# Kernel tuning notes

Hardware: AMD Instinct MI355X
Metric: run time of the kernel (lower is better)

## Reference

```python
import jax, jax.numpy as jnp
import numpy as np

NV = [156, 618, 2466]     # vertices per ellipsoid level
NE = [462, 1848, 7392]    # edges per level
NGT = 30000               # ground-truth point-cloud size
LAP_CONST = [0.2, 1.0, 1.0]


def setup_inputs() -> dict:
    key = jax.random.key(0)
    ks = jax.random.split(key, 20)
    inp = {"points": jax.random.normal(ks[0], (1, NGT, 3), jnp.float32)}
    for i, (n, e) in enumerate(zip(NV, NE)):
        inp[f"pred_coord_{i}"] = jax.random.normal(ks[1 + i], (n, 3), jnp.float32)
        inp[f"pbd_{i}"] = jax.random.normal(ks[4 + i], (n, 3), jnp.float32)
        inp[f"edges_{i}"] = jax.random.randint(ks[7 + i], (e, 2), 0, n)
        # laplace_idx layout: 8 neighbor ids (-1 padded), vertex id, valence
        nbr = jax.random.randint(ks[10 + i], (n, 8), 0, n)
        drop = jax.random.uniform(ks[13 + i], (n, 8)) < 0.2
        drop = drop.at[:, 0].set(False)  # keep valence >= 1
        nbr = jnp.where(drop, -1, nbr)
        deg = (nbr >= 0).sum(1)
        inp[f"lap_idx_{i}"] = jnp.concatenate(
            [nbr, jnp.arange(n)[:, None], deg[:, None]], axis=1)
    return inp


def chamfer(gt, pred):
    # gt: [B, Ng, 3], pred: [B, Np, 3] -> squared NN distances each way
    d = (jnp.sum(gt * gt, -1)[:, :, None]
         + jnp.sum(pred * pred, -1)[:, None, :]
         - 2.0 * jnp.einsum('bnd,bmd->bnm', gt, pred))  # [B, Ng, Np]
    return jnp.min(d, axis=2), jnp.min(d, axis=1)


def edge_regularization(pred, edges):
    edge = pred[edges[:, 0]] - pred[edges[:, 1]]
    return jnp.mean(jnp.sum(edge * edge, axis=1)) * 300.0


def laplace_coord(x, lap_idx):
    nbr = lap_idx[:, :8]
    valid = nbr >= 0
    v = jnp.where(valid[:, :, None], x[jnp.clip(nbr, 0)], 0.0)  # [N, 8, 3]
    deg = lap_idx[:, -1].astype(x.dtype)
    return x - v.sum(1) / deg[:, None]


def laplace_regularization(x_before, x_after, lap_idx, use_move):
    lap1 = laplace_coord(x_before, lap_idx)
    lap2 = laplace_coord(x_after, lap_idx)
    d = lap1 - lap2
    loss = jnp.mean(d * d) * 3.0  # MSE over [N,3] scaled by last dim
    if use_move:
        m = x_before - x_after
        loss = loss + jnp.mean(m * m) * 3.0
    return loss


def reference(points, pred_coord_0, pred_coord_1, pred_coord_2,
              pbd_0, pbd_1, pbd_2,
              edges_0, edges_1, edges_2,
              lap_idx_0, lap_idx_1, lap_idx_2):
    pred_coord = [pred_coord_0, pred_coord_1, pred_coord_2]
    pbd = [pbd_0, pbd_1, pbd_2]
    edges = [edges_0, edges_1, edges_2]
    lap_idx = [lap_idx_0, lap_idx_1, lap_idx_2]

    chamfer_loss = 0.0
    edge_loss = 0.0
    lap_loss = 0.0
    for i in range(3):
        dist1, dist2 = chamfer(points, pbd[i][None])
        chamfer_loss = chamfer_loss + jnp.mean(dist1) + jnp.mean(dist2)
        edge_loss = edge_loss + edge_regularization(pred_coord[i], edges[i])
        lap_loss = lap_loss + LAP_CONST[i] * laplace_regularization(
            pbd[i], pred_coord[i], lap_idx[i], i > 0)
    loss = 100.0 * chamfer_loss + 0.1 * edge_loss + 0.3 * lap_loss
    return loss, chamfer_loss, edge_loss, lap_loss
```

## Files before the change

kernel.cpp:

```cpp
#include <hip/hip_runtime.h>

#define NGT 30000
#define GT_TILE 1024
#define NBLK_G 30
#define CHUNK 128
#define NCHUNK 27
#define RB 128

__global__ __launch_bounds__(256) void chamfer_kernel(
    const float* __restrict__ gt,
    const float* __restrict__ pbd0,
    const float* __restrict__ pbd1,
    const float* __restrict__ pbd2,
    float* __restrict__ gtmin,
    float* __restrict__ predmin)
{
    __shared__ float4 sgt[GT_TILE];
    __shared__ float4 spred[CHUNK];

    const int tid = threadIdx.x;
    const int c = blockIdx.y;

    int mesh, cidx;
    if (c < 2)      { mesh = 0; cidx = c; }
    else if (c < 7) { mesh = 1; cidx = c - 2; }
    else            { mesh = 2; cidx = c - 7; }
    const int coff = cidx * CHUNK;
    const int n    = (mesh == 0) ? 156 : (mesh == 1) ? 618 : 2466;
    const int poff = (mesh == 0) ? 0   : (mesh == 1) ? 156 : 774;
    const float* pred = (mesh == 0) ? pbd0 : (mesh == 1) ? pbd1 : pbd2;
    const int np = min(CHUNK, n - coff);

    if (tid < CHUNK) {
        float4 v = make_float4(0.f, 0.f, 0.f, 0.f);
        if (tid < np) {
            const int j = coff + tid;
            float px = pred[3*j], py = pred[3*j+1], pz = pred[3*j+2];
            v = make_float4(px, py, pz, px*px + py*py + pz*pz);
        }
        spred[tid] = v;
    }

    const int gbase = blockIdx.x * GT_TILE;
    float gx[4], gy[4], gz[4], g2[4], gmin[4];
    #pragma unroll
    for (int k = 0; k < 4; ++k) {
        const int g = gbase + k * 256 + tid;
        float x = 1e18f, y = 1e18f, z = 1e18f;
        if (g < NGT) { x = gt[3*g]; y = gt[3*g+1]; z = gt[3*g+2]; }
        gx[k] = x; gy[k] = y; gz[k] = z;
        g2[k] = x*x + y*y + z*z;
        gmin[k] = 3.0e38f;
        sgt[k * 256 + tid] = make_float4(x, y, z, g2[k]);
    }
    __syncthreads();

    #pragma unroll 2
    for (int j = 0; j < np; ++j) {
        const float4 p = spred[j];
        #pragma unroll
        for (int k = 0; k < 4; ++k) {
            float dot = gx[k]*p.x + gy[k]*p.y + gz[k]*p.z;
            float t = __fmaf_rn(dot, -2.0f, p.w);
            gmin[k] = fminf(gmin[k], t);
        }
    }
    #pragma unroll
    for (int k = 0; k < 4; ++k) {
        const int g = gbase + k * 256 + tid;
        if (g < NGT)
            atomicMin((int*)(gtmin + mesh * NGT + g),
                      __float_as_int(gmin[k] + g2[k]));
    }

    {
        const int grp = tid >> 3;
        const int s   = tid & 7;
        float4 p[4];
        #pragma unroll
        for (int r = 0; r < 4; ++r) p[r] = spred[4*grp + r];
        float mn[4] = {3.0e38f, 3.0e38f, 3.0e38f, 3.0e38f};
        #pragma unroll 2
        for (int k = 0; k < GT_TILE / 8; ++k) {
            const float4 q = sgt[k * 8 + s];
            #pragma unroll
            for (int r = 0; r < 4; ++r) {
                float dot = q.x*p[r].x + q.y*p[r].y + q.z*p[r].z;
                float t = __fmaf_rn(dot, -2.0f, q.w);
                mn[r] = fminf(mn[r], t);
            }
        }
        #pragma unroll
        for (int off = 1; off < 8; off <<= 1) {
            #pragma unroll
            for (int r = 0; r < 4; ++r)
                mn[r] = fminf(mn[r], __shfl_xor(mn[r], off, 64));
        }
        if (s == 0) {
            #pragma unroll
            for (int r = 0; r < 4; ++r) {
                const int pj = 4*grp + r;
                if (pj < np)
                    atomicMin((int*)(predmin + poff + coff + pj),
                              __float_as_int(mn[r] + p[r].w));
            }
        }
    }
}

__global__ __launch_bounds__(256) void partial_kernel(
    const float* __restrict__ pc0, const float* __restrict__ pc1, const float* __restrict__ pc2,
    const float* __restrict__ pbd0, const float* __restrict__ pbd1, const float* __restrict__ pbd2,
    const int* __restrict__ ed0, const int* __restrict__ ed1, const int* __restrict__ ed2,
    const int* __restrict__ li0, const int* __restrict__ li1, const int* __restrict__ li2,
    const float* __restrict__ gtmin, const float* __restrict__ predmin,
    float* __restrict__ partials)
{
    const int   NVs[3]   = {156, 618, 2466};
    const int   NEs[3]   = {462, 1848, 7392};
    const int   poffs[3] = {0, 156, 774};
    const int   eoffs[3] = {0, 462, 2310};
    const float lapc[3]  = {0.2f, 1.0f, 1.0f};
    const float* pcs[3]  = {pc0, pc1, pc2};
    const float* pbds[3] = {pbd0, pbd1, pbd2};
    const int*   eds[3]  = {ed0, ed1, ed2};
    const int*   lis[3]  = {li0, li1, li2};

    const int tid = threadIdx.x;
    const int stride = gridDim.x * 256;
    float ch = 0.f, ed = 0.f, lp = 0.f;

    for (int idx = blockIdx.x * 256 + tid; idx < 106182; idx += stride) {
        if (idx < 90000) {
            ch += gtmin[idx] * (1.0f / 30000.0f);
        } else if (idx < 93240) {
            int p = idx - 90000;
            int m = (p < 156) ? 0 : (p < 774) ? 1 : 2;
            ch += predmin[p] * (1.0f / (float)NVs[m]);
        } else if (idx < 102942) {
            int e = idx - 93240;
            int m = (e < 462) ? 0 : (e < 2310) ? 1 : 2;
            int el = e - eoffs[m];
            const int* E = eds[m];
            const float* P = pcs[m];
            int a = E[2*el], b = E[2*el+1];
            float dx = P[3*a]   - P[3*b];
            float dy = P[3*a+1] - P[3*b+1];
            float dz = P[3*a+2] - P[3*b+2];
            ed += (dx*dx + dy*dy + dz*dz) * (300.0f / (float)NEs[m]);
        } else {
            int v = idx - 102942;
            int m = (v < 156) ? 0 : (v < 774) ? 1 : 2;
            int vl = v - poffs[m];
            const int* L = lis[m];
            const float* PB = pbds[m];
            const float* PC = pcs[m];
            float mvx = PB[3*vl]   - PC[3*vl];
            float mvy = PB[3*vl+1] - PC[3*vl+1];
            float mvz = PB[3*vl+2] - PC[3*vl+2];
            float sx = 0.f, sy = 0.f, sz = 0.f;
            #pragma unroll
            for (int k = 0; k < 8; ++k) {
                int nb = L[10*vl + k];
                if (nb >= 0) {
                    sx += PB[3*nb]   - PC[3*nb];
                    sy += PB[3*nb+1] - PC[3*nb+1];
                    sz += PB[3*nb+2] - PC[3*nb+2];
                }
            }
            float invdeg = 1.0f / (float)L[10*vl + 9];
            float dx = mvx - sx * invdeg;
            float dy = mvy - sy * invdeg;
            float dz = mvz - sz * invdeg;
            float t = dx*dx + dy*dy + dz*dz;
            if (m > 0) t += mvx*mvx + mvy*mvy + mvz*mvz;
            lp += t * (lapc[m] / (float)NVs[m]);
        }
    }

    __shared__ float sred[12];
    for (int off = 32; off; off >>= 1) {
        ch += __shfl_down(ch, off, 64);
        ed += __shfl_down(ed, off, 64);
        lp += __shfl_down(lp, off, 64);
    }
    const int lane = tid & 63, wid = tid >> 6;
    if (lane == 0) { sred[wid] = ch; sred[4 + wid] = ed; sred[8 + wid] = lp; }
    __syncthreads();
    if (tid == 0) {
        partials[blockIdx.x * 4 + 0] = sred[0] + sred[1] + sred[2] + sred[3];
        partials[blockIdx.x * 4 + 1] = sred[4] + sred[5] + sred[6] + sred[7];
        partials[blockIdx.x * 4 + 2] = sred[8] + sred[9] + sred[10] + sred[11];
    }
}

__global__ __launch_bounds__(128) void final_kernel(
    const float* __restrict__ partials, float* __restrict__ out)
{
    const int tid = threadIdx.x;
    float ch = partials[4*tid], ed = partials[4*tid+1], lp = partials[4*tid+2];
    __shared__ float s[6];
    for (int off = 32; off; off >>= 1) {
        ch += __shfl_down(ch, off, 64);
        ed += __shfl_down(ed, off, 64);
        lp += __shfl_down(lp, off, 64);
    }
    if ((tid & 63) == 0) {
        int w = tid >> 6;
        s[w] = ch; s[2 + w] = ed; s[4 + w] = lp;
    }
    __syncthreads();
    if (tid == 0) {
        float c = s[0] + s[1], e = s[2] + s[3], l = s[4] + s[5];
        out[0] = 100.0f * c + 0.1f * e + 0.3f * l;
        out[1] = c;
        out[2] = e;
        out[3] = l;
    }
}

extern "C" void kernel_launch(void* const* d_in, const int* in_sizes, int n_in,
                              void* d_out, int out_size, void* d_ws, size_t ws_size,
                              hipStream_t stream) {
    const float* gt   = (const float*)d_in[0];
    const float* pc0  = (const float*)d_in[1];
    const float* pbd0 = (const float*)d_in[2];
    const int*   ed0  = (const int*)  d_in[3];
    const int*   li0  = (const int*)  d_in[4];
    const float* pc1  = (const float*)d_in[5];
    const float* pbd1 = (const float*)d_in[6];
    const int*   ed1  = (const int*)  d_in[7];
    const int*   li1  = (const int*)  d_in[8];
    const float* pc2  = (const float*)d_in[9];
    const float* pbd2 = (const float*)d_in[10];
    const int*   ed2  = (const int*)  d_in[11];
    const int*   li2  = (const int*)  d_in[12];

    float* ws       = (float*)d_ws;
    float* gtmin    = ws;
    float* predmin  = ws + 3 * NGT;
    float* partials = ws + 3 * NGT + 3240;
    float* out      = (float*)d_out;

    hipMemsetAsync(gtmin, 0x7f, (3 * NGT + 3240) * sizeof(float), stream);

    dim3 grid(NBLK_G, NCHUNK);
    chamfer_kernel<<<grid, 256, 0, stream>>>(gt, pbd0, pbd1, pbd2, gtmin, predmin);

    partial_kernel<<<RB, 256, 0, stream>>>(pc0, pc1, pc2, pbd0, pbd1, pbd2,
                                           ed0, ed1, ed2, li0, li1, li2,
                                           gtmin, predmin, partials);

    final_kernel<<<1, 128, 0, stream>>>(partials, out);
}
```

Measured before the change: 53.50 us.

## Compute chamfer distances once and reduce pred-side minima with shuffle transpose

Each gt-pred distance is now computed once and used for both directions. The per-gt minimum is kept in registers. The per-pred minimum is reduced across the wavefront with a butterfly shuffle-transpose, so lane j ends up holding pred j's minimum. This removes the second shared-memory pass over the gt tile and the sgt buffer. The chunk size drops to 64 so the 64-entry per-thread array fits a wavefront, at the cost of more register pressure and twice as many gt-side atomics.

```diff
diff --git a/kernel.cpp b/kernel.cpp
--- a/kernel.cpp
+++ b/kernel.cpp
@@ -3,8 +3,8 @@
 #define NGT 30000
 #define GT_TILE 1024
 #define NBLK_G 30
-#define CHUNK 128
-#define NCHUNK 27
+#define CHUNK 64
+#define NCHUNK 52
 #define RB 128
 
 __global__ __launch_bounds__(256) void chamfer_kernel(
@@ -15,16 +15,15 @@
     float* __restrict__ gtmin,
     float* __restrict__ predmin)
 {
-    __shared__ float4 sgt[GT_TILE];
     __shared__ float4 spred[CHUNK];
 
     const int tid = threadIdx.x;
     const int c = blockIdx.y;
 
     int mesh, cidx;
-    if (c < 2)      { mesh = 0; cidx = c; }
-    else if (c < 7) { mesh = 1; cidx = c - 2; }
-    else            { mesh = 2; cidx = c - 7; }
+    if (c < 3)       { mesh = 0; cidx = c; }
+    else if (c < 13) { mesh = 1; cidx = c - 3; }
+    else             { mesh = 2; cidx = c - 13; }
     const int coff = cidx * CHUNK;
     const int n    = (mesh == 0) ? 156 : (mesh == 1) ? 618 : 2466;
     const int poff = (mesh == 0) ? 0   : (mesh == 1) ? 156 : 774;
@@ -32,7 +31,7 @@
     const int np = min(CHUNK, n - coff);
 
     if (tid < CHUNK) {
-        float4 v = make_float4(0.f, 0.f, 0.f, 0.f);
+        float4 v = make_float4(0.f, 0.f, 0.f, 3.0e38f);
         if (tid < np) {
             const int j = coff + tid;
             float px = pred[3*j], py = pred[3*j+1], pz = pred[3*j+2];
@@ -51,60 +50,67 @@
         gx[k] = x; gy[k] = y; gz[k] = z;
         g2[k] = x*x + y*y + z*z;
         gmin[k] = 3.0e38f;
-        sgt[k * 256 + tid] = make_float4(x, y, z, g2[k]);
     }
     __syncthreads();
 
-    #pragma unroll 2
-    for (int j = 0; j < np; ++j) {
+    float pm[CHUNK];
+    #pragma unroll
+    for (int j = 0; j < CHUNK; ++j) {
         const float4 p = spred[j];
+        float d[4];
         #pragma unroll
         for (int k = 0; k < 4; ++k) {
             float dot = gx[k]*p.x + gy[k]*p.y + gz[k]*p.z;
             float t = __fmaf_rn(dot, -2.0f, p.w);
-            gmin[k] = fminf(gmin[k], t);
+            d[k] = t + g2[k];
+            gmin[k] = fminf(gmin[k], d[k]);
         }
-    }
+        pm[j] = fminf(fminf(d[0], d[1]), fminf(d[2], d[3]));
+    }
+
     #pragma unroll
     for (int k = 0; k < 4; ++k) {
         const int g = gbase + k * 256 + tid;
         if (g < NGT)
-            atomicMin((int*)(gtmin + mesh * NGT + g),
-                      __float_as_int(gmin[k] + g2[k]));
-    }
-
+            atomicMin((int*)(gtmin + mesh * NGT + g), __float_as_int(gmin[k]));
+    }
+
+    const int lane = tid & 63;
+    float r32[32];
+    #pragma unroll
+    for (int j = 0; j < 32; ++j) {
+        float a = (lane & 32) ? pm[j + 32] : pm[j];
+        r32[j] = fminf(a, __shfl_xor(a, 32, 64));
+    }
+    float r16[16];
+    #pragma unroll
+    for (int j = 0; j < 16; ++j) {
+        float a = (lane & 16) ? r32[j + 16] : r32[j];
+        r16[j] = fminf(a, __shfl_xor(a, 16, 64));
+    }
+    float r8[8];
+    #pragma unroll
+    for (int j = 0; j < 8; ++j) {
+        float a = (lane & 8) ? r16[j + 8] : r16[j];
+        r8[j] = fminf(a, __shfl_xor(a, 8, 64));
+    }
+    float r4[4];
+    #pragma unroll
+    for (int j = 0; j < 4; ++j) {
+        float a = (lane & 4) ? r8[j + 4] : r8[j];
+        r4[j] = fminf(a, __shfl_xor(a, 4, 64));
+    }
+    float r2[2];
+    #pragma unroll
+    for (int j = 0; j < 2; ++j) {
+        float a = (lane & 2) ? r4[j + 2] : r4[j];
+        r2[j] = fminf(a, __shfl_xor(a, 2, 64));
+    }
     {
-        const int grp = tid >> 3;
-        const int s   = tid & 7;
-        float4 p[4];
-        #pragma unroll
-        for (int r = 0; r < 4; ++r) p[r] = spred[4*grp + r];
-        float mn[4] = {3.0e38f, 3.0e38f, 3.0e38f, 3.0e38f};
-        #pragma unroll 2
-        for (int k = 0; k < GT_TILE / 8; ++k) {
-            const float4 q = sgt[k * 8 + s];
-            #pragma unroll
-            for (int r = 0; r < 4; ++r) {
-                float dot = q.x*p[r].x + q.y*p[r].y + q.z*p[r].z;
-                float t = __fmaf_rn(dot, -2.0f, q.w);
-                mn[r] = fminf(mn[r], t);
-            }
-        }
-        #pragma unroll
-        for (int off = 1; off < 8; off <<= 1) {
-            #pragma unroll
-            for (int r = 0; r < 4; ++r)
-                mn[r] = fminf(mn[r], __shfl_xor(mn[r], off, 64));
-        }
-        if (s == 0) {
-            #pragma unroll
-            for (int r = 0; r < 4; ++r) {
-                const int pj = 4*grp + r;
-                if (pj < np)
-                    atomicMin((int*)(predmin + poff + coff + pj),
-                              __float_as_int(mn[r] + p[r].w));
-            }
-        }
+        float a = (lane & 1) ? r2[1] : r2[0];
+        float r = fminf(a, __shfl_xor(a, 1, 64));
+        if (lane < np)
+            atomicMin((int*)(predmin + poff + coff + lane), __float_as_int(r));
     }
 }
 
```

After: 87.05 us. 62.7% more time.
